# Optimization experiments

Measured on AMD Instinct MI355X. Metric: run time of the kernel, lower is better.

The kernel has to match this reference:

```python
import jax, jax.numpy as jnp
import numpy as np

D_V, D_Q, D_H = 256, 128, 64

def setup_inputs() -> dict:
    key = jax.random.key(0)
    ks = jax.random.split(key, 8)
    B, T = 512, 512
    query = jax.random.normal(ks[0], (B, D_Q), dtype=jnp.float32)
    values = jax.random.normal(ks[1], (B, T, D_V), dtype=jnp.float32)
    s1 = 1.0 / np.sqrt(D_V)
    s2 = 1.0 / np.sqrt(D_Q)
    sv = 1.0 / np.sqrt(D_H)
    W1 = jax.random.uniform(ks[2], (D_H, D_V), jnp.float32, -s1, s1)
    b1 = jax.random.uniform(ks[3], (D_H,), jnp.float32, -s1, s1)
    W2 = jax.random.uniform(ks[4], (D_H, D_Q), jnp.float32, -s2, s2)
    b2 = jax.random.uniform(ks[5], (D_H,), jnp.float32, -s2, s2)
    Wv = jax.random.uniform(ks[6], (1, D_H), jnp.float32, -sv, sv)
    bv = jax.random.uniform(ks[7], (1,), jnp.float32, -sv, sv)
    return {"query": query, "values": values, "W1": W1, "b1": b1,
            "W2": W2, "b2": b2, "Wv": Wv, "bv": bv}

def reference(query, values, W1, b1, W2, b2, Wv, bv):
    # hidden_with_time_axis: [B,1,128]
    h = jnp.einsum('btv,hv->bth', values, W1) + b1 \
        + (jnp.einsum('bq,hq->bh', query, W2) + b2)[:, None, :]   # [B,T,64]
    score = jnp.einsum('bth,oh->bto', jnp.tanh(h), Wv) + bv        # [B,T,1]
    attention_weights = jax.nn.softmax(score, axis=0)              # softmax over dim 0, as written
    context_vector = jnp.sum(attention_weights * values, axis=0)   # [T,256]
    return (context_vector, attention_weights)
```

## Files before the change

### kernel.cpp

```cpp
#include <hip/hip_runtime.h>
#include <hip/hip_bf16.h>

#define Tt 512
#define Bb 512
#define DV 256
#define DQ 128
#define DH 64
#define CTXN (Tt * DV)

typedef __attribute__((ext_vector_type(8))) short bf16x8;
typedef __attribute__((ext_vector_type(4))) float f32x4;

__device__ __forceinline__ unsigned short f2bf(float x) {
  unsigned u = __float_as_uint(x);
  u += 0x7FFFu + ((u >> 16) & 1u);
  return (unsigned short)(u >> 16);
}

__global__ void qh_kernel(const float* __restrict__ query,
                          const float* __restrict__ W2,
                          const float* __restrict__ b1,
                          const float* __restrict__ b2,
                          float* __restrict__ qh) {
  int b = blockIdx.x;
  int h = threadIdx.x;
  __shared__ float q[DQ];
  q[h]      = query[b * DQ + h];
  q[h + 64] = query[b * DQ + h + 64];
  __syncthreads();
  const float* w2r = W2 + h * DQ;
  float acc = 0.f;
#pragma unroll 8
  for (int k = 0; k < DQ; ++k) acc = fmaf(w2r[k], q[k], acc);
  qh[b * DH + h] = acc + b1[h] + b2[h];
}

__global__ void w1_cvt_kernel(const float* __restrict__ W1,
                              unsigned short* __restrict__ w1bf) {
  int i = blockIdx.x * 256 + threadIdx.x;
  w1bf[i] = f2bf(W1[i]);
}

__global__ __launch_bounds__(256, 4) void score_kernel(
    const float* __restrict__ values,
    const unsigned short* __restrict__ w1bf,
    const float* __restrict__ qh,
    const float* __restrict__ Wv,
    const float* __restrict__ bv,
    float* __restrict__ sT) {
  __shared__ __align__(16) unsigned short lB[DH * DV];
  const int tid = threadIdx.x;
  const int m0 = blockIdx.x * 64;
  const int bidx = m0 >> 9;

  const uint4* w1v = (const uint4*)w1bf;
#pragma unroll
  for (int i = 0; i < 8; ++i) {
    int vec = i * 256 + tid;
    uint4 d = w1v[vec];
    int row = vec >> 5;
    int u = vec & 31;
    int byte = (row << 9) + (u << 4);
    *(uint4*)((char*)lB + (byte ^ ((row & 7) << 4))) = d;
  }
  __syncthreads();

  const int wv = tid >> 6;
  const int lane = tid & 63;
  const int lrow = lane & 15;
  const int g = lane >> 4;

  f32x4 acc[4];
#pragma unroll
  for (int nt = 0; nt < 4; ++nt) acc[nt] = (f32x4){0.f, 0.f, 0.f, 0.f};

  const int arow = wv * 16 + lrow;
  const float* ap = values + (size_t)(m0 + arow) * DV;

#pragma unroll
  for (int ks = 0; ks < 8; ++ks) {
    const float* fp = ap + ks * 32 + g * 8;
    float4 f0 = *(const float4*)(fp);
    float4 f1 = *(const float4*)(fp + 4);
    bf16x8 af;
    af[0] = (short)f2bf(f0.x); af[1] = (short)f2bf(f0.y);
    af[2] = (short)f2bf(f0.z); af[3] = (short)f2bf(f0.w);
    af[4] = (short)f2bf(f1.x); af[5] = (short)f2bf(f1.y);
    af[6] = (short)f2bf(f1.z); af[7] = (short)f2bf(f1.w);
    int k2 = (ks * 32 + g * 8) * 2;
#pragma unroll
    for (int nt = 0; nt < 4; ++nt) {
      int brow = nt * 16 + lrow;
      bf16x8 bf = *(const bf16x8*)((const char*)lB +
                                   (((brow << 9) + k2) ^ ((brow & 7) << 4)));
      acc[nt] = __builtin_amdgcn_mfma_f32_16x16x32_bf16(af, bf, acc[nt], 0, 0, 0);
    }
  }

  float bv0 = bv[0];
  float sc[4] = {0.f, 0.f, 0.f, 0.f};
#pragma unroll
  for (int nt = 0; nt < 4; ++nt) {
    int col = nt * 16 + lrow;
    float qv = qh[bidx * DH + col];
    float wvc = Wv[col];
#pragma unroll
    for (int j = 0; j < 4; ++j) {
      float hv = acc[nt][j] + qv;
      float e = __expf(2.f * hv);
      float th = (e - 1.f) / (e + 1.f);
      sc[j] = fmaf(th, wvc, sc[j]);
    }
  }
#pragma unroll
  for (int j = 0; j < 4; ++j) {
    float v = sc[j];
    v += __shfl_xor(v, 1);
    v += __shfl_xor(v, 2);
    v += __shfl_xor(v, 4);
    v += __shfl_xor(v, 8);
    sc[j] = v;
  }
  if (lrow == 0) {
#pragma unroll
    for (int j = 0; j < 4; ++j) {
      int m = m0 + wv * 16 + g * 4 + j;
      int tt = m & (Tt - 1);
      sT[tt * Bb + bidx] = sc[j] + bv0;
    }
  }
}

__global__ __launch_bounds__(1024, 8) void ctx_kernel(
    const float* __restrict__ values,
    const float* __restrict__ sT,
    float* __restrict__ out) {
  const int t = blockIdx.x;
  const int tid = threadIdx.x;
  const int wv = tid >> 6, lane = tid & 63;
  __shared__ float wbuf[Bb];
  __shared__ float smax[16], ssum[16];
  __shared__ float4 cred[16][64];

  float s = -1e30f;
  if (tid < Bb) s = sT[t * Bb + tid];
  float mx = s;
#pragma unroll
  for (int d = 1; d < 64; d <<= 1) mx = fmaxf(mx, __shfl_xor(mx, d));
  if (lane == 0) smax[wv] = mx;
  __syncthreads();
  mx = smax[0];
#pragma unroll
  for (int i = 1; i < 16; ++i) mx = fmaxf(mx, smax[i]);
  float w = (tid < Bb) ? __expf(s - mx) : 0.f;
  float zs = w;
#pragma unroll
  for (int d = 1; d < 64; d <<= 1) zs += __shfl_xor(zs, d);
  if (lane == 0) ssum[wv] = zs;
  __syncthreads();
  float Z = 0.f;
#pragma unroll
  for (int i = 0; i < 16; ++i) Z += ssum[i];
  float wn = w / Z;
  if (tid < Bb) {
    wbuf[tid] = wn;
    out[CTXN + tid * Tt + t] = wn;
  }
  __syncthreads();

  const float4* vp = (const float4*)values;
  size_t base = ((size_t)wv * Tt + t) * (DV / 4) + lane;
  const size_t stride = (size_t)16 * Tt * (DV / 4);
  float4 acc = make_float4(0.f, 0.f, 0.f, 0.f);
#pragma unroll 4
  for (int i = 0; i < 32; ++i) {
    float4 v = vp[base];
    base += stride;
    float wb = wbuf[wv + (i << 4)];
    acc.x = fmaf(wb, v.x, acc.x);
    acc.y = fmaf(wb, v.y, acc.y);
    acc.z = fmaf(wb, v.z, acc.z);
    acc.w = fmaf(wb, v.w, acc.w);
  }
  cred[wv][lane] = acc;
  __syncthreads();
  if (wv == 0) {
    float4 tot = cred[0][lane];
#pragma unroll
    for (int i = 1; i < 16; ++i) {
      float4 a = cred[i][lane];
      tot.x += a.x; tot.y += a.y; tot.z += a.z; tot.w += a.w;
    }
    ((float4*)out)[t * (DV / 4) + lane] = tot;
  }
}

extern "C" void kernel_launch(void* const* d_in, const int* in_sizes, int n_in,
                              void* d_out, int out_size, void* d_ws, size_t ws_size,
                              hipStream_t stream) {
  const float* query  = (const float*)d_in[0];
  const float* values = (const float*)d_in[1];
  const float* W1     = (const float*)d_in[2];
  const float* b1     = (const float*)d_in[3];
  const float* W2     = (const float*)d_in[4];
  const float* b2     = (const float*)d_in[5];
  const float* Wv     = (const float*)d_in[6];
  const float* bv     = (const float*)d_in[7];
  float* out = (float*)d_out;
  char* ws = (char*)d_ws;
  float* qh            = (float*)ws;
  unsigned short* w1bf = (unsigned short*)(ws + 131072);
  float* sT            = (float*)(ws + 131072 + 32768);

  hipLaunchKernelGGL(qh_kernel, dim3(Bb), dim3(DH), 0, stream, query, W2, b1, b2, qh);
  hipLaunchKernelGGL(w1_cvt_kernel, dim3(64), dim3(256), 0, stream, W1, w1bf);
  hipLaunchKernelGGL(score_kernel, dim3((Bb * Tt) / 64), dim3(256), 0, stream,
                     values, w1bf, qh, Wv, bv, sT);
  hipLaunchKernelGGL(ctx_kernel, dim3(Tt), dim3(1024), 0, stream, values, sT, out);
}
```

Measured before the change: 103.2 us.

## Store bf16 transposed values copy in score pass and reduce context from it

The score kernel now writes the bf16-converted values it already computes into a workspace buffer laid out as [T][B][DV]. A new context kernel reads this half-size, contiguous-per-t buffer instead of strided fp32 values. The qh and W1-conversion kernels are also merged into one launch. The change trades an extra write of half the values tensor for a smaller, coalesced second read. It also lowers context precision to bf16 inputs and only runs if the workspace is large enough.

```diff
diff --git a/kernel.cpp b/kernel.cpp
--- a/kernel.cpp
+++ b/kernel.cpp
@@ -7,8 +7,10 @@
 #define DQ 128
 #define DH 64
 #define CTXN (Tt * DV)
+#define VBF_BYTES ((size_t)Bb * Tt * DV * 2)
 
 typedef __attribute__((ext_vector_type(8))) short bf16x8;
+typedef __attribute__((ext_vector_type(8))) unsigned short u16x8;
 typedef __attribute__((ext_vector_type(4))) float f32x4;
 
 __device__ __forceinline__ unsigned short f2bf(float x) {
@@ -16,42 +18,53 @@
   u += 0x7FFFu + ((u >> 16) & 1u);
   return (unsigned short)(u >> 16);
 }
-
-__global__ void qh_kernel(const float* __restrict__ query,
-                          const float* __restrict__ W2,
-                          const float* __restrict__ b1,
-                          const float* __restrict__ b2,
-                          float* __restrict__ qh) {
-  int b = blockIdx.x;
-  int h = threadIdx.x;
+__device__ __forceinline__ float bf2f(unsigned short b) {
+  return __uint_as_float(((unsigned)b) << 16);
+}
+
+__global__ void prep_kernel(const float* __restrict__ query,
+                            const float* __restrict__ W1,
+                            const float* __restrict__ W2,
+                            const float* __restrict__ b1,
+                            const float* __restrict__ b2,
+                            float* __restrict__ qh,
+                            unsigned short* __restrict__ w1bf) {
   __shared__ float q[DQ];
-  q[h]      = query[b * DQ + h];
-  q[h + 64] = query[b * DQ + h + 64];
-  __syncthreads();
-  const float* w2r = W2 + h * DQ;
-  float acc = 0.f;
+  const int blk = blockIdx.x;
+  const int h = threadIdx.x;
+  if (blk < Bb) {
+    q[h]      = query[blk * DQ + h];
+    q[h + 64] = query[blk * DQ + h + 64];
+    __syncthreads();
+    const float* w2r = W2 + h * DQ;
+    float acc = 0.f;
 #pragma unroll 8
-  for (int k = 0; k < DQ; ++k) acc = fmaf(w2r[k], q[k], acc);
-  qh[b * DH + h] = acc + b1[h] + b2[h];
-}
-
-__global__ void w1_cvt_kernel(const float* __restrict__ W1,
-                              unsigned short* __restrict__ w1bf) {
-  int i = blockIdx.x * 256 + threadIdx.x;
-  w1bf[i] = f2bf(W1[i]);
-}
-
+    for (int k = 0; k < DQ; ++k) acc = fmaf(w2r[k], q[k], acc);
+    qh[blk * DH + h] = acc + b1[h] + b2[h];
+  } else {
+    int base = (blk - Bb) * 256;
+#pragma unroll
+    for (int k = 0; k < 4; ++k) {
+      int i = base + (k << 6) + h;
+      w1bf[i] = f2bf(W1[i]);
+    }
+  }
+}
+
+template <bool WRITEV>
 __global__ __launch_bounds__(256, 4) void score_kernel(
     const float* __restrict__ values,
     const unsigned short* __restrict__ w1bf,
     const float* __restrict__ qh,
     const float* __restrict__ Wv,
     const float* __restrict__ bv,
-    float* __restrict__ sT) {
+    float* __restrict__ sT,
+    unsigned short* __restrict__ vbfT) {
   __shared__ __align__(16) unsigned short lB[DH * DV];
   const int tid = threadIdx.x;
   const int m0 = blockIdx.x * 64;
   const int bidx = m0 >> 9;
+  const int t0 = m0 & (Tt - 1);
 
   const uint4* w1v = (const uint4*)w1bf;
 #pragma unroll
@@ -76,6 +89,9 @@
 
   const int arow = wv * 16 + lrow;
   const float* ap = values + (size_t)(m0 + arow) * DV;
+  unsigned short* vst = WRITEV
+      ? vbfT + ((size_t)(t0 + arow) * Bb + bidx) * DV + g * 8
+      : nullptr;
 
 #pragma unroll
   for (int ks = 0; ks < 8; ++ks) {
@@ -87,6 +103,7 @@
     af[2] = (short)f2bf(f0.z); af[3] = (short)f2bf(f0.w);
     af[4] = (short)f2bf(f1.x); af[5] = (short)f2bf(f1.y);
     af[6] = (short)f2bf(f1.z); af[7] = (short)f2bf(f1.w);
+    if (WRITEV) *(bf16x8*)(vst + ks * 32) = af;
     int k2 = (ks * 32 + g * 8) * 2;
 #pragma unroll
     for (int nt = 0; nt < 4; ++nt) {
@@ -131,7 +148,67 @@
   }
 }
 
-__global__ __launch_bounds__(1024, 8) void ctx_kernel(
+__global__ __launch_bounds__(1024) void ctx_bf_kernel(
+    const unsigned short* __restrict__ vbfT,
+    const float* __restrict__ sT,
+    float* __restrict__ out) {
+  const int t = blockIdx.x;
+  const int tid = threadIdx.x;
+  const int wv = tid >> 6, lane = tid & 63;
+  __shared__ float wbuf[Bb];
+  __shared__ float smax[16], ssum[16];
+  __shared__ float red[32][DV];
+
+  float s = -1e30f;
+  if (tid < Bb) s = sT[t * Bb + tid];
+  float mx = s;
+#pragma unroll
+  for (int d = 1; d < 64; d <<= 1) mx = fmaxf(mx, __shfl_xor(mx, d));
+  if (lane == 0) smax[wv] = mx;
+  __syncthreads();
+  mx = smax[0];
+#pragma unroll
+  for (int i = 1; i < 16; ++i) mx = fmaxf(mx, smax[i]);
+  float w = (tid < Bb) ? __expf(s - mx) : 0.f;
+  float zs = w;
+#pragma unroll
+  for (int d = 1; d < 64; d <<= 1) zs += __shfl_xor(zs, d);
+  if (lane == 0) ssum[wv] = zs;
+  __syncthreads();
+  float Z = 0.f;
+#pragma unroll
+  for (int i = 0; i < 16; ++i) Z += ssum[i];
+  float wn = w / Z;
+  if (tid < Bb) {
+    wbuf[tid] = wn;
+    out[CTXN + tid * Tt + t] = wn;
+  }
+  __syncthreads();
+
+  const u16x8* vp = (const u16x8*)(vbfT + (size_t)t * Bb * DV);
+  const int unit = tid & 31;
+  const int b0 = tid >> 5;
+  float av[8] = {0.f, 0.f, 0.f, 0.f, 0.f, 0.f, 0.f, 0.f};
+#pragma unroll 4
+  for (int i = 0; i < 16; ++i) {
+    int b = (i << 5) + b0;
+    u16x8 v = vp[(b << 5) + unit];
+    float wb = wbuf[b];
+#pragma unroll
+    for (int j = 0; j < 8; ++j) av[j] = fmaf(wb, bf2f(v[j]), av[j]);
+  }
+#pragma unroll
+  for (int j = 0; j < 8; ++j) red[b0][unit * 8 + j] = av[j];
+  __syncthreads();
+  if (tid < DV) {
+    float tot = 0.f;
+#pragma unroll
+    for (int b = 0; b < 32; ++b) tot += red[b][tid];
+    out[t * DV + tid] = tot;
+  }
+}
+
+__global__ __launch_bounds__(1024) void ctx_kernel(
     const float* __restrict__ values,
     const float* __restrict__ sT,
     float* __restrict__ out) {
@@ -210,11 +287,18 @@
   char* ws = (char*)d_ws;
   float* qh            = (float*)ws;
   unsigned short* w1bf = (unsigned short*)(ws + 131072);
-  float* sT            = (float*)(ws + 131072 + 32768);
-
-  hipLaunchKernelGGL(qh_kernel, dim3(Bb), dim3(DH), 0, stream, query, W2, b1, b2, qh);
-  hipLaunchKernelGGL(w1_cvt_kernel, dim3(64), dim3(256), 0, stream, W1, w1bf);
-  hipLaunchKernelGGL(score_kernel, dim3((Bb * Tt) / 64), dim3(256), 0, stream,
-                     values, w1bf, qh, Wv, bv, sT);
-  hipLaunchKernelGGL(ctx_kernel, dim3(Tt), dim3(1024), 0, stream, values, sT, out);
-}
+  float* sT            = (float*)(ws + 163840);
+  unsigned short* vbfT = (unsigned short*)(ws + (size_t)2 * 1024 * 1024);
+  const bool use_bf = ws_size >= (size_t)2 * 1024 * 1024 + VBF_BYTES;
+
+  prep_kernel<<<dim3(Bb + 64), dim3(64), 0, stream>>>(query, W1, W2, b1, b2, qh, w1bf);
+  if (use_bf) {
+    score_kernel<true><<<dim3((Bb * Tt) / 64), dim3(256), 0, stream>>>(
+        values, w1bf, qh, Wv, bv, sT, vbfT);
+    ctx_bf_kernel<<<dim3(Tt), dim3(1024), 0, stream>>>(vbfT, sT, out);
+  } else {
+    score_kernel<false><<<dim3((Bb * Tt) / 64), dim3(256), 0, stream>>>(
+        values, w1bf, qh, Wv, bv, sT, nullptr);
+    ctx_kernel<<<dim3(Tt), dim3(1024), 0, stream>>>(values, sT, out);
+  }
+}
```

Result: slower. 112.9 us (+9.4%).

## Fuse score and context passes into a single streaming pass over values

Applied to the files above, without the earlier changes.

Scoring and weighted context accumulation now happen in one kernel. Each block computes exp(score) for a 16-timestep by 32-batch tile and immediately accumulates exp-weighted bf16 values into per-wave partial numerators and denominators. Separate finalize kernels then reduce the 64 partials per timestep and normalize the attention weights. The goal is to read the large values tensor once instead of twice. In exchange it drops the max-subtraction in the softmax (safe only because scores are bounded), accumulates the context from bf16-rounded values, adds about 32MB of partial-sum traffic, and runs at low occupancy with a large register footprint. The two small prep kernels are also merged into one launch.

```diff
diff --git a/kernel.cpp b/kernel.cpp
--- a/kernel.cpp
+++ b/kernel.cpp
@@ -16,42 +16,54 @@
   u += 0x7FFFu + ((u >> 16) & 1u);
   return (unsigned short)(u >> 16);
 }
-
-__global__ void qh_kernel(const float* __restrict__ query,
-                          const float* __restrict__ W2,
-                          const float* __restrict__ b1,
-                          const float* __restrict__ b2,
-                          float* __restrict__ qh) {
-  int b = blockIdx.x;
-  int h = threadIdx.x;
+__device__ __forceinline__ float bf2f(unsigned short b) {
+  return __uint_as_float(((unsigned)b) << 16);
+}
+
+__global__ void prep_kernel(const float* __restrict__ query,
+                            const float* __restrict__ W1,
+                            const float* __restrict__ W2,
+                            const float* __restrict__ b1,
+                            const float* __restrict__ b2,
+                            float* __restrict__ qh,
+                            unsigned short* __restrict__ w1bf) {
   __shared__ float q[DQ];
-  q[h]      = query[b * DQ + h];
-  q[h + 64] = query[b * DQ + h + 64];
-  __syncthreads();
-  const float* w2r = W2 + h * DQ;
-  float acc = 0.f;
+  const int blk = blockIdx.x;
+  const int h = threadIdx.x;
+  if (blk < Bb) {
+    q[h]      = query[blk * DQ + h];
+    q[h + 64] = query[blk * DQ + h + 64];
+    __syncthreads();
+    const float* w2r = W2 + h * DQ;
+    float acc = 0.f;
 #pragma unroll 8
-  for (int k = 0; k < DQ; ++k) acc = fmaf(w2r[k], q[k], acc);
-  qh[b * DH + h] = acc + b1[h] + b2[h];
-}
-
-__global__ void w1_cvt_kernel(const float* __restrict__ W1,
-                              unsigned short* __restrict__ w1bf) {
-  int i = blockIdx.x * 256 + threadIdx.x;
-  w1bf[i] = f2bf(W1[i]);
-}
-
-__global__ __launch_bounds__(256, 4) void score_kernel(
+    for (int k = 0; k < DQ; ++k) acc = fmaf(w2r[k], q[k], acc);
+    qh[blk * DH + h] = acc + b1[h] + b2[h];
+  } else {
+    int base = (blk - Bb) * 256;
+#pragma unroll
+    for (int k = 0; k < 4; ++k) {
+      int i = base + (k << 6) + h;
+      w1bf[i] = f2bf(W1[i]);
+    }
+  }
+}
+
+__global__ __launch_bounds__(256, 2) void fused_kernel(
     const float* __restrict__ values,
     const unsigned short* __restrict__ w1bf,
     const float* __restrict__ qh,
     const float* __restrict__ Wv,
     const float* __restrict__ bv,
-    float* __restrict__ sT) {
+    float* __restrict__ es,
+    float* __restrict__ num_p,
+    float* __restrict__ den_p) {
   __shared__ __align__(16) unsigned short lB[DH * DV];
+  __shared__ float lQh[32 * DH];
   const int tid = threadIdx.x;
-  const int m0 = blockIdx.x * 64;
-  const int bidx = m0 >> 9;
+  const int bcid = blockIdx.x & 15;
+  const int t0 = (blockIdx.x >> 4) * 16;
+  const int bbase = bcid * 32;
 
   const uint4* w1v = (const uint4*)w1bf;
 #pragma unroll
@@ -63,135 +75,134 @@
     int byte = (row << 9) + (u << 4);
     *(uint4*)((char*)lB + (byte ^ ((row & 7) << 4))) = d;
   }
+#pragma unroll
+  for (int i = 0; i < 8; ++i)
+    lQh[i * 256 + tid] = qh[bbase * DH + i * 256 + tid];
   __syncthreads();
 
-  const int wv = tid >> 6;
-  const int lane = tid & 63;
-  const int lrow = lane & 15;
-  const int g = lane >> 4;
-
-  f32x4 acc[4];
-#pragma unroll
-  for (int nt = 0; nt < 4; ++nt) acc[nt] = (f32x4){0.f, 0.f, 0.f, 0.f};
-
-  const int arow = wv * 16 + lrow;
-  const float* ap = values + (size_t)(m0 + arow) * DV;
-
+  const int wv = tid >> 6, lane = tid & 63;
+  const int lrow = lane & 15, g = lane >> 4;
+
+  float wvc[4];
+#pragma unroll
+  for (int nt = 0; nt < 4; ++nt) wvc[nt] = Wv[nt * 16 + lrow];
+  const float bv0 = bv[0];
+
+  float num[8][8];
+#pragma unroll
+  for (int ks = 0; ks < 8; ++ks)
+#pragma unroll
+    for (int e = 0; e < 8; ++e) num[ks][e] = 0.f;
+  float den = 0.f;
+
+#pragma unroll 2
+  for (int i = 0; i < 8; ++i) {
+    const int b = bbase + wv * 8 + i;
+    const float* ap = values + ((size_t)b * Tt + t0 + lrow) * DV + g * 8;
+
+    bf16x8 af[8];
+#pragma unroll
+    for (int ks = 0; ks < 8; ++ks) {
+      float4 f0 = *(const float4*)(ap + ks * 32);
+      float4 f1 = *(const float4*)(ap + ks * 32 + 4);
+      af[ks][0] = (short)f2bf(f0.x); af[ks][1] = (short)f2bf(f0.y);
+      af[ks][2] = (short)f2bf(f0.z); af[ks][3] = (short)f2bf(f0.w);
+      af[ks][4] = (short)f2bf(f1.x); af[ks][5] = (short)f2bf(f1.y);
+      af[ks][6] = (short)f2bf(f1.z); af[ks][7] = (short)f2bf(f1.w);
+    }
+
+    f32x4 acc[4];
+#pragma unroll
+    for (int nt = 0; nt < 4; ++nt) acc[nt] = (f32x4){0.f, 0.f, 0.f, 0.f};
+#pragma unroll
+    for (int ks = 0; ks < 8; ++ks) {
+      int k2 = (ks * 32 + g * 8) * 2;
+#pragma unroll
+      for (int nt = 0; nt < 4; ++nt) {
+        int brow = nt * 16 + lrow;
+        bf16x8 bf = *(const bf16x8*)((const char*)lB +
+                                     (((brow << 9) + k2) ^ ((brow & 7) << 4)));
+        acc[nt] = __builtin_amdgcn_mfma_f32_16x16x32_bf16(af[ks], bf, acc[nt], 0, 0, 0);
+      }
+    }
+
+    const float* qrow = lQh + (wv * 8 + i) * DH;
+    float sc[4] = {0.f, 0.f, 0.f, 0.f};
+#pragma unroll
+    for (int nt = 0; nt < 4; ++nt) {
+      float qv = qrow[nt * 16 + lrow];
+#pragma unroll
+      for (int j = 0; j < 4; ++j) {
+        float hv = acc[nt][j] + qv;
+        float e2 = __expf(2.f * hv);
+        float th = (e2 - 1.f) / (e2 + 1.f);
+        sc[j] = fmaf(th, wvc[nt], sc[j]);
+      }
+    }
+#pragma unroll
+    for (int j = 0; j < 4; ++j) {
+      float v = sc[j];
+      v += __shfl_xor(v, 1);
+      v += __shfl_xor(v, 2);
+      v += __shfl_xor(v, 4);
+      v += __shfl_xor(v, 8);
+      sc[j] = __expf(v + bv0);
+    }
+    if (lrow == 0) {
+#pragma unroll
+      for (int j = 0; j < 4; ++j)
+        es[(size_t)b * Tt + t0 + g * 4 + j] = sc[j];
+    }
+    int src = (lrow >> 2) << 4;
+    float w0 = __shfl(sc[0], src), w1 = __shfl(sc[1], src);
+    float w2 = __shfl(sc[2], src), w3 = __shfl(sc[3], src);
+    int jm = lrow & 3;
+    float w = (jm == 0) ? w0 : (jm == 1) ? w1 : (jm == 2) ? w2 : w3;
+    den += w;
+#pragma unroll
+    for (int ks = 0; ks < 8; ++ks)
+#pragma unroll
+      for (int e = 0; e < 8; ++e)
+        num[ks][e] = fmaf(w, bf2f((unsigned short)af[ks][e]), num[ks][e]);
+  }
+
+  const int wc = bcid * 4 + wv;
+  float* np = num_p + ((size_t)wc * Tt + t0 + lrow) * DV + g * 8;
 #pragma unroll
   for (int ks = 0; ks < 8; ++ks) {
-    const float* fp = ap + ks * 32 + g * 8;
-    float4 f0 = *(const float4*)(fp);
-    float4 f1 = *(const float4*)(fp + 4);
-    bf16x8 af;
-    af[0] = (short)f2bf(f0.x); af[1] = (short)f2bf(f0.y);
-    af[2] = (short)f2bf(f0.z); af[3] = (short)f2bf(f0.w);
-    af[4] = (short)f2bf(f1.x); af[5] = (short)f2bf(f1.y);
-    af[6] = (short)f2bf(f1.z); af[7] = (short)f2bf(f1.w);
-    int k2 = (ks * 32 + g * 8) * 2;
-#pragma unroll
-    for (int nt = 0; nt < 4; ++nt) {
-      int brow = nt * 16 + lrow;
-      bf16x8 bf = *(const bf16x8*)((const char*)lB +
-                                   (((brow << 9) + k2) ^ ((brow & 7) << 4)));
-      acc[nt] = __builtin_amdgcn_mfma_f32_16x16x32_bf16(af, bf, acc[nt], 0, 0, 0);
-    }
-  }
-
-  float bv0 = bv[0];
-  float sc[4] = {0.f, 0.f, 0.f, 0.f};
-#pragma unroll
-  for (int nt = 0; nt < 4; ++nt) {
-    int col = nt * 16 + lrow;
-    float qv = qh[bidx * DH + col];
-    float wvc = Wv[col];
-#pragma unroll
-    for (int j = 0; j < 4; ++j) {
-      float hv = acc[nt][j] + qv;
-      float e = __expf(2.f * hv);
-      float th = (e - 1.f) / (e + 1.f);
-      sc[j] = fmaf(th, wvc, sc[j]);
-    }
-  }
-#pragma unroll
-  for (int j = 0; j < 4; ++j) {
-    float v = sc[j];
-    v += __shfl_xor(v, 1);
-    v += __shfl_xor(v, 2);
-    v += __shfl_xor(v, 4);
-    v += __shfl_xor(v, 8);
-    sc[j] = v;
-  }
-  if (lrow == 0) {
-#pragma unroll
-    for (int j = 0; j < 4; ++j) {
-      int m = m0 + wv * 16 + g * 4 + j;
-      int tt = m & (Tt - 1);
-      sT[tt * Bb + bidx] = sc[j] + bv0;
-    }
-  }
-}
-
-__global__ __launch_bounds__(1024, 8) void ctx_kernel(
-    const float* __restrict__ values,
-    const float* __restrict__ sT,
-    float* __restrict__ out) {
+    *(float4*)(np + ks * 32) =
+        make_float4(num[ks][0], num[ks][1], num[ks][2], num[ks][3]);
+    *(float4*)(np + ks * 32 + 4) =
+        make_float4(num[ks][4], num[ks][5], num[ks][6], num[ks][7]);
+  }
+  if (g == 0) den_p[wc * Tt + t0 + lrow] = den;
+}
+
+__global__ __launch_bounds__(256) void fin_ctx_kernel(
+    const float* __restrict__ num_p, const float* __restrict__ den_p,
+    float* __restrict__ Zbuf, float* __restrict__ out) {
   const int t = blockIdx.x;
   const int tid = threadIdx.x;
-  const int wv = tid >> 6, lane = tid & 63;
-  __shared__ float wbuf[Bb];
-  __shared__ float smax[16], ssum[16];
-  __shared__ float4 cred[16][64];
-
-  float s = -1e30f;
-  if (tid < Bb) s = sT[t * Bb + tid];
-  float mx = s;
-#pragma unroll
-  for (int d = 1; d < 64; d <<= 1) mx = fmaxf(mx, __shfl_xor(mx, d));
-  if (lane == 0) smax[wv] = mx;
-  __syncthreads();
-  mx = smax[0];
-#pragma unroll
-  for (int i = 1; i < 16; ++i) mx = fmaxf(mx, smax[i]);
-  float w = (tid < Bb) ? __expf(s - mx) : 0.f;
-  float zs = w;
-#pragma unroll
-  for (int d = 1; d < 64; d <<= 1) zs += __shfl_xor(zs, d);
-  if (lane == 0) ssum[wv] = zs;
-  __syncthreads();
   float Z = 0.f;
-#pragma unroll
-  for (int i = 0; i < 16; ++i) Z += ssum[i];
-  float wn = w / Z;
-  if (tid < Bb) {
-    wbuf[tid] = wn;
-    out[CTXN + tid * Tt + t] = wn;
-  }
-  __syncthreads();
-
-  const float4* vp = (const float4*)values;
-  size_t base = ((size_t)wv * Tt + t) * (DV / 4) + lane;
-  const size_t stride = (size_t)16 * Tt * (DV / 4);
-  float4 acc = make_float4(0.f, 0.f, 0.f, 0.f);
-#pragma unroll 4
-  for (int i = 0; i < 32; ++i) {
-    float4 v = vp[base];
-    base += stride;
-    float wb = wbuf[wv + (i << 4)];
-    acc.x = fmaf(wb, v.x, acc.x);
-    acc.y = fmaf(wb, v.y, acc.y);
-    acc.z = fmaf(wb, v.z, acc.z);
-    acc.w = fmaf(wb, v.w, acc.w);
-  }
-  cred[wv][lane] = acc;
-  __syncthreads();
-  if (wv == 0) {
-    float4 tot = cred[0][lane];
-#pragma unroll
-    for (int i = 1; i < 16; ++i) {
-      float4 a = cred[i][lane];
-      tot.x += a.x; tot.y += a.y; tot.z += a.z; tot.w += a.w;
-    }
-    ((float4*)out)[t * (DV / 4) + lane] = tot;
+#pragma unroll 16
+  for (int w = 0; w < 64; ++w) Z += den_p[w * Tt + t];
+  float s = 0.f;
+#pragma unroll 8
+  for (int w = 0; w < 64; ++w)
+    s += num_p[((size_t)w * Tt + t) * DV + tid];
+  out[t * DV + tid] = s / Z;
+  if (tid == 0) Zbuf[t] = Z;
+}
+
+__global__ __launch_bounds__(256) void fin_w_kernel(
+    const float* __restrict__ es, const float* __restrict__ Zbuf,
+    float* __restrict__ out) {
+  const int b = blockIdx.x;
+  const int tid = threadIdx.x;
+#pragma unroll
+  for (int i = 0; i < 2; ++i) {
+    int t = i * 256 + tid;
+    out[CTXN + b * Tt + t] = es[(size_t)b * Tt + t] / Zbuf[t];
   }
 }
 
@@ -210,11 +221,14 @@
   char* ws = (char*)d_ws;
   float* qh            = (float*)ws;
   unsigned short* w1bf = (unsigned short*)(ws + 131072);
-  float* sT            = (float*)(ws + 131072 + 32768);
-
-  hipLaunchKernelGGL(qh_kernel, dim3(Bb), dim3(DH), 0, stream, query, W2, b1, b2, qh);
-  hipLaunchKernelGGL(w1_cvt_kernel, dim3(64), dim3(256), 0, stream, W1, w1bf);
-  hipLaunchKernelGGL(score_kernel, dim3((Bb * Tt) / 64), dim3(256), 0, stream,
-                     values, w1bf, qh, Wv, bv, sT);
-  hipLaunchKernelGGL(ctx_kernel, dim3(Tt), dim3(1024), 0, stream, values, sT, out);
-}
+  float* es            = (float*)(ws + 163840);
+  float* den_p         = (float*)(ws + 1212416);
+  float* Zbuf          = (float*)(ws + 1343488);
+  float* num_p         = (float*)(ws + 1345536);
+
+  prep_kernel<<<dim3(Bb + 64), dim3(64), 0, stream>>>(query, W1, W2, b1, b2, qh, w1bf);
+  fused_kernel<<<dim3(512), dim3(256), 0, stream>>>(values, w1bf, qh, Wv, bv,
+                                                    es, num_p, den_p);
+  fin_ctx_kernel<<<dim3(Tt), dim3(256), 0, stream>>>(num_p, den_p, Zbuf, out);
+  fin_w_kernel<<<dim3(Bb), dim3(256), 0, stream>>>(es, Zbuf, out);
+}
```

Result: slower. 184.0 us (+78.3%).

## Stash bf16 copy of values in score pass and read it in context pass

Applied to the files above, without the earlier changes.

The score kernel now writes the bf16-rounded values it already builds for the MFMA into a workspace buffer. When the workspace is large enough, the context kernel reads that half-size copy instead of the fp32 values, aiming to cut the bytes fetched in the second pass. Other changes: the score kernel stores exp(score) directly, which drops the softmax max-subtraction; the qh and W1 conversion kernels are merged into one launch; and the context reduction is re-tiled. Costs and risks: an extra 128MB write, bf16 rounding in the context accumulation, and possible overflow from the unshifted exp.

```diff
diff --git a/kernel.cpp b/kernel.cpp
--- a/kernel.cpp
+++ b/kernel.cpp
@@ -7,8 +7,10 @@
 #define DQ 128
 #define DH 64
 #define CTXN (Tt * DV)
+#define VBF_BYTES ((size_t)Bb * Tt * DV * 2)
 
 typedef __attribute__((ext_vector_type(8))) short bf16x8;
+typedef __attribute__((ext_vector_type(8))) unsigned short u16x8;
 typedef __attribute__((ext_vector_type(4))) float f32x4;
 
 __device__ __forceinline__ unsigned short f2bf(float x) {
@@ -16,38 +18,48 @@
   u += 0x7FFFu + ((u >> 16) & 1u);
   return (unsigned short)(u >> 16);
 }
-
-__global__ void qh_kernel(const float* __restrict__ query,
-                          const float* __restrict__ W2,
-                          const float* __restrict__ b1,
-                          const float* __restrict__ b2,
-                          float* __restrict__ qh) {
-  int b = blockIdx.x;
-  int h = threadIdx.x;
+__device__ __forceinline__ float bf2f(unsigned short b) {
+  return __uint_as_float(((unsigned)b) << 16);
+}
+
+__global__ void prep_kernel(const float* __restrict__ query,
+                            const float* __restrict__ W1,
+                            const float* __restrict__ W2,
+                            const float* __restrict__ b1,
+                            const float* __restrict__ b2,
+                            float* __restrict__ qh,
+                            unsigned short* __restrict__ w1bf) {
   __shared__ float q[DQ];
-  q[h]      = query[b * DQ + h];
-  q[h + 64] = query[b * DQ + h + 64];
-  __syncthreads();
-  const float* w2r = W2 + h * DQ;
-  float acc = 0.f;
+  const int blk = blockIdx.x;
+  const int h = threadIdx.x;
+  if (blk < Bb) {
+    q[h]      = query[blk * DQ + h];
+    q[h + 64] = query[blk * DQ + h + 64];
+    __syncthreads();
+    const float* w2r = W2 + h * DQ;
+    float acc = 0.f;
 #pragma unroll 8
-  for (int k = 0; k < DQ; ++k) acc = fmaf(w2r[k], q[k], acc);
-  qh[b * DH + h] = acc + b1[h] + b2[h];
-}
-
-__global__ void w1_cvt_kernel(const float* __restrict__ W1,
-                              unsigned short* __restrict__ w1bf) {
-  int i = blockIdx.x * 256 + threadIdx.x;
-  w1bf[i] = f2bf(W1[i]);
-}
-
-__global__ __launch_bounds__(256, 4) void score_kernel(
+    for (int k = 0; k < DQ; ++k) acc = fmaf(w2r[k], q[k], acc);
+    qh[blk * DH + h] = acc + b1[h] + b2[h];
+  } else {
+    int base = (blk - Bb) * 256;
+#pragma unroll
+    for (int k = 0; k < 4; ++k) {
+      int i = base + (k << 6) + h;
+      w1bf[i] = f2bf(W1[i]);
+    }
+  }
+}
+
+template <bool WRITEV>
+__global__ __launch_bounds__(256, 4) void score2_kernel(
     const float* __restrict__ values,
     const unsigned short* __restrict__ w1bf,
     const float* __restrict__ qh,
     const float* __restrict__ Wv,
     const float* __restrict__ bv,
-    float* __restrict__ sT) {
+    float* __restrict__ esT,
+    unsigned short* __restrict__ vbf) {
   __shared__ __align__(16) unsigned short lB[DH * DV];
   const int tid = threadIdx.x;
   const int m0 = blockIdx.x * 64;
@@ -76,6 +88,9 @@
 
   const int arow = wv * 16 + lrow;
   const float* ap = values + (size_t)(m0 + arow) * DV;
+  unsigned short* vst = WRITEV
+      ? vbf + (size_t)(m0 + arow) * DV + g * 8
+      : nullptr;
 
 #pragma unroll
   for (int ks = 0; ks < 8; ++ks) {
@@ -87,6 +102,7 @@
     af[2] = (short)f2bf(f0.z); af[3] = (short)f2bf(f0.w);
     af[4] = (short)f2bf(f1.x); af[5] = (short)f2bf(f1.y);
     af[6] = (short)f2bf(f1.z); af[7] = (short)f2bf(f1.w);
+    if (WRITEV) *(bf16x8*)(vst + ks * 32) = af;
     int k2 = (ks * 32 + g * 8) * 2;
 #pragma unroll
     for (int nt = 0; nt < 4; ++nt) {
@@ -126,72 +142,67 @@
     for (int j = 0; j < 4; ++j) {
       int m = m0 + wv * 16 + g * 4 + j;
       int tt = m & (Tt - 1);
-      sT[tt * Bb + bidx] = sc[j] + bv0;
-    }
-  }
-}
-
-__global__ __launch_bounds__(1024, 8) void ctx_kernel(
+      esT[tt * Bb + bidx] = __expf(sc[j] + bv0);
+    }
+  }
+}
+
+__global__ __launch_bounds__(1024, 2) void ctx2_kernel(
     const float* __restrict__ values,
-    const float* __restrict__ sT,
+    const unsigned short* __restrict__ vbf,
+    const float* __restrict__ esT,
+    int use_bf,
     float* __restrict__ out) {
   const int t = blockIdx.x;
   const int tid = threadIdx.x;
   const int wv = tid >> 6, lane = tid & 63;
   __shared__ float wbuf[Bb];
-  __shared__ float smax[16], ssum[16];
-  __shared__ float4 cred[16][64];
-
-  float s = -1e30f;
-  if (tid < Bb) s = sT[t * Bb + tid];
-  float mx = s;
-#pragma unroll
-  for (int d = 1; d < 64; d <<= 1) mx = fmaxf(mx, __shfl_xor(mx, d));
-  if (lane == 0) smax[wv] = mx;
-  __syncthreads();
-  mx = smax[0];
-#pragma unroll
-  for (int i = 1; i < 16; ++i) mx = fmaxf(mx, smax[i]);
-  float w = (tid < Bb) ? __expf(s - mx) : 0.f;
-  float zs = w;
+  __shared__ float ssum[16];
+  __shared__ float red[32][DV];
+
+  float es = (tid < Bb) ? esT[t * Bb + tid] : 0.f;
+  float zs = es;
 #pragma unroll
   for (int d = 1; d < 64; d <<= 1) zs += __shfl_xor(zs, d);
   if (lane == 0) ssum[wv] = zs;
+  if (tid < Bb) wbuf[tid] = es;
   __syncthreads();
   float Z = 0.f;
 #pragma unroll
   for (int i = 0; i < 16; ++i) Z += ssum[i];
-  float wn = w / Z;
-  if (tid < Bb) {
-    wbuf[tid] = wn;
-    out[CTXN + tid * Tt + t] = wn;
-  }
+  const float invZ = 1.f / Z;
+  if (tid < Bb)
+    out[CTXN + tid * Tt + t] = es * invZ;
+
+  const int unit = tid & 31;
+  const int brow = tid >> 5;
+  float av[8] = {0.f, 0.f, 0.f, 0.f, 0.f, 0.f, 0.f, 0.f};
+#pragma unroll 4
+  for (int i = 0; i < 16; ++i) {
+    int b = (i << 5) + brow;
+    float w = wbuf[b];
+    if (use_bf) {
+      u16x8 v = *(const u16x8*)(vbf + ((size_t)b * Tt + t) * DV + unit * 8);
+#pragma unroll
+      for (int j = 0; j < 8; ++j) av[j] = fmaf(w, bf2f(v[j]), av[j]);
+    } else {
+      const float* p = values + ((size_t)b * Tt + t) * DV + unit * 8;
+      float4 a = ((const float4*)p)[0];
+      float4 c = ((const float4*)p)[1];
+      av[0] = fmaf(w, a.x, av[0]); av[1] = fmaf(w, a.y, av[1]);
+      av[2] = fmaf(w, a.z, av[2]); av[3] = fmaf(w, a.w, av[3]);
+      av[4] = fmaf(w, c.x, av[4]); av[5] = fmaf(w, c.y, av[5]);
+      av[6] = fmaf(w, c.z, av[6]); av[7] = fmaf(w, c.w, av[7]);
+    }
+  }
+#pragma unroll
+  for (int j = 0; j < 8; ++j) red[brow][unit * 8 + j] = av[j];
   __syncthreads();
-
-  const float4* vp = (const float4*)values;
-  size_t base = ((size_t)wv * Tt + t) * (DV / 4) + lane;
-  const size_t stride = (size_t)16 * Tt * (DV / 4);
-  float4 acc = make_float4(0.f, 0.f, 0.f, 0.f);
-#pragma unroll 4
-  for (int i = 0; i < 32; ++i) {
-    float4 v = vp[base];
-    base += stride;
-    float wb = wbuf[wv + (i << 4)];
-    acc.x = fmaf(wb, v.x, acc.x);
-    acc.y = fmaf(wb, v.y, acc.y);
-    acc.z = fmaf(wb, v.z, acc.z);
-    acc.w = fmaf(wb, v.w, acc.w);
-  }
-  cred[wv][lane] = acc;
-  __syncthreads();
-  if (wv == 0) {
-    float4 tot = cred[0][lane];
-#pragma unroll
-    for (int i = 1; i < 16; ++i) {
-      float4 a = cred[i][lane];
-      tot.x += a.x; tot.y += a.y; tot.z += a.z; tot.w += a.w;
-    }
-    ((float4*)out)[t * (DV / 4) + lane] = tot;
+  if (tid < DV) {
+    float tot = 0.f;
+#pragma unroll
+    for (int b = 0; b < 32; ++b) tot += red[b][tid];
+    out[t * DV + tid] = tot * invZ;
   }
 }
 
@@ -210,11 +221,18 @@
   char* ws = (char*)d_ws;
   float* qh            = (float*)ws;
   unsigned short* w1bf = (unsigned short*)(ws + 131072);
-  float* sT            = (float*)(ws + 131072 + 32768);
-
-  hipLaunchKernelGGL(qh_kernel, dim3(Bb), dim3(DH), 0, stream, query, W2, b1, b2, qh);
-  hipLaunchKernelGGL(w1_cvt_kernel, dim3(64), dim3(256), 0, stream, W1, w1bf);
-  hipLaunchKernelGGL(score_kernel, dim3((Bb * Tt) / 64), dim3(256), 0, stream,
-                     values, w1bf, qh, Wv, bv, sT);
-  hipLaunchKernelGGL(ctx_kernel, dim3(Tt), dim3(1024), 0, stream, values, sT, out);
-}
+  float* esT           = (float*)(ws + 163840);
+  unsigned short* vbf  = (unsigned short*)(ws + (size_t)2 * 1024 * 1024);
+  const bool use_bf = ws_size >= (size_t)2 * 1024 * 1024 + VBF_BYTES;
+
+  prep_kernel<<<dim3(Bb + 64), dim3(64), 0, stream>>>(query, W1, W2, b1, b2, qh, w1bf);
+  if (use_bf) {
+    score2_kernel<true><<<dim3((Bb * Tt) / 64), dim3(256), 0, stream>>>(
+        values, w1bf, qh, Wv, bv, esT, vbf);
+    ctx2_kernel<<<dim3(Tt), dim3(1024), 0, stream>>>(values, vbf, esT, 1, out);
+  } else {
+    score2_kernel<false><<<dim3((Bb * Tt) / 64), dim3(256), 0, stream>>>(
+        values, w1bf, qh, Wv, bv, esT, nullptr);
+    ctx2_kernel<<<dim3(Tt), dim3(1024), 0, stream>>>(values, nullptr, esT, 0, out);
+  }
+}
```

After: 111.7 us. 1.08x slower.
